# Kernel tuning notes

Hardware: AMD Instinct MI355X
Metric: run time of the kernel (lower is better)

## Reference

```python
import jax, jax.numpy as jnp
import numpy as np
from jax.scipy.linalg import expm

LATENT, HIDDEN, N_PARTS, K = 128, 2048, 128, 2048
OMEGA_DIM, TRANZ_DIM = 9 * N_PARTS, 3 * N_PARTS


def setup_inputs() -> dict:
    key = jax.random.key(0)
    ks = jax.random.split(key, 10)

    def w(k, out_d, in_d):
        # eqx.nn.Linear-style scale ~ 1/sqrt(fan_in)
        return jax.random.normal(k, (out_d, in_d), dtype=jnp.float32) / np.sqrt(in_d)

    return {
        "x_init": jax.random.normal(ks[0], (LATENT, K), dtype=jnp.float32),
        "Wo0": w(ks[1], HIDDEN, LATENT),
        "Wo1": w(ks[2], HIDDEN, HIDDEN),
        "Wo2": w(ks[3], HIDDEN, HIDDEN),
        "Wo3": w(ks[4], OMEGA_DIM, HIDDEN),
        "Wt0": w(ks[5], HIDDEN, LATENT),
        "Wt1": w(ks[6], HIDDEN, HIDDEN),
        "Wt2": w(ks[7], HIDDEN, HIDDEN),
        "Wt3": w(ks[8], TRANZ_DIM, HIDDEN),
    }


def _mlp(weights, x):
    # bias-free MLP, relu on all but last layer; x is (d_in, K)
    for i, W in enumerate(weights):
        x = W @ x
        if i + 1 < len(weights):
            x = jax.nn.relu(x)
    return x


def reference(x_init, Wo0, Wo1, Wo2, Wo3, Wt0, Wt1, Wt2, Wt3):
    omega = _mlp([Wo0, Wo1, Wo2, Wo3], x_init)            # (9n, K)
    n = omega.shape[0] // 9
    k = omega.shape[1]
    # exp_omega 2D branch: vmap over columns, each column -> (n,3,3) expm batch
    mats = omega.T.reshape(k * n, 3, 3)
    R = jax.vmap(expm)(mats).reshape(k, 9 * n)            # (K, 9n)
    rotations = R.T                                        # (9n, K)
    translations = _mlp([Wt0, Wt1, Wt2, Wt3], x_init)     # (3n, K)
    # form_transformations (2D branch): stack translation as a 4th row -> (12n, K)
    rot_r = rotations.reshape(n, 3, 3, k)
    tr_r = translations.reshape(n, 1, 3, k)
    transf = jnp.concatenate([rot_r, tr_r], axis=1).reshape(-1, k)  # (12n, K)
    return (omega, transf, rotations, translations)
```

## Files before the change

### kernel.cpp

```cpp
#include <hip/hip_runtime.h>
#include <stdint.h>


typedef short bf16x8 __attribute__((ext_vector_type(8)));
typedef float f32x4 __attribute__((ext_vector_type(4)));

__device__ __forceinline__ unsigned short f2bf(float f) {
  unsigned int x = __float_as_uint(f);
  unsigned int r = (x + 0x7fffu + ((x >> 16) & 1u)) >> 16;
  return (unsigned short)r;
}

__device__ __forceinline__ void gld_lds16(const void* g, void* l) {
  __builtin_amdgcn_global_load_lds(
      (__attribute__((address_space(1))) void*)(g),
      (__attribute__((address_space(3))) void*)(l),
      16, 0, 0);
}

__device__ __forceinline__ unsigned lds_addr(const void* p) {
  return (unsigned)(uintptr_t)(__attribute__((address_space(3))) const void*)p;
}

__device__ __forceinline__ bf16x8 ds_read128(unsigned a) {
  bf16x8 r;
  asm volatile("ds_read_b128 %0, %1" : "=v"(r) : "v"(a));
  return r;
}

#define ASM_BAR asm volatile("s_barrier" ::: "memory")
#define LGKM0   asm volatile("s_waitcnt lgkmcnt(0)" ::: "memory")
#define VMCNT0  asm volatile("s_waitcnt vmcnt(0)" ::: "memory")
#define SCHED0  __builtin_amdgcn_sched_barrier(0)

__global__ void prep_k(const float* __restrict__ x,
                       const float* __restrict__ wo0, const float* __restrict__ wo1,
                       const float* __restrict__ wo2, const float* __restrict__ wo3,
                       const float* __restrict__ wt0, const float* __restrict__ wt1,
                       const float* __restrict__ wt2, const float* __restrict__ wt3,
                       unsigned short* __restrict__ dst, unsigned short* __restrict__ xt) {
  __shared__ float tile[32][33];
  const int b = blockIdx.x;
  const int tid = threadIdx.x;
  if (b >= 9984) {
    const int r = b - 9984;
    const int bx = r & 63, by = r >> 6;
    const int tx = tid & 31, ty = tid >> 5;
#pragma unroll
    for (int i = 0; i < 32; i += 8)
      tile[ty + i][tx] = x[(size_t)(by * 32 + ty + i) * 2048 + bx * 32 + tx];
    __syncthreads();
#pragma unroll
    for (int i = 0; i < 32; i += 8)
      xt[(size_t)(bx * 32 + ty + i) * 128 + by * 32 + tx] = f2bf(tile[tx][ty + i]);
    return;
  }
  int idx = (b * 256 + tid) * 8;
  if (idx >= 20447232) return;
  const float* src;
  int off;
  if (idx < 8650752) {
    if (idx < 262144)       { src = wo0; off = idx; }
    else if (idx < 4456448) { src = wo1; off = idx - 262144; }
    else                    { src = wo2; off = idx - 4456448; }
  } else {
    if (idx < 11010048)      { src = wo3; off = idx - 8650752; }
    else if (idx < 11272192) { src = wt0; off = idx - 11010048; }
    else if (idx < 15466496) { src = wt1; off = idx - 11272192; }
    else if (idx < 19660800) { src = wt2; off = idx - 15466496; }
    else                     { src = wt3; off = idx - 19660800; }
  }
  float4 a = *(const float4*)(src + off);
  float4 c = *(const float4*)(src + off + 4);
  uint4 o;
  o.x = (unsigned)f2bf(a.x) | ((unsigned)f2bf(a.y) << 16);
  o.y = (unsigned)f2bf(a.z) | ((unsigned)f2bf(a.w) << 16);
  o.z = (unsigned)f2bf(c.x) | ((unsigned)f2bf(c.y) << 16);
  o.w = (unsigned)f2bf(c.z) | ((unsigned)f2bf(c.w) << 16);
  *(uint4*)(dst + idx) = o;
}

template <int SWZ>
__global__ __launch_bounds__(256, 2) void gemm_tn(
    const unsigned short* __restrict__ A0, const unsigned short* __restrict__ B0,
    unsigned short* __restrict__ C0, int n0tiles, int ldc0,
    const unsigned short* __restrict__ A1, const unsigned short* __restrict__ B1,
    unsigned short* __restrict__ C1, int ldc1, int K) {
  __shared__ alignas(16) unsigned short Asl[128 * 128];
  __shared__ alignas(16) unsigned short Bsl[128 * 128];

  int mt, yt;
  if (SWZ) {
    int id = blockIdx.x;
    int xcd = id & 7, s = id >> 3;
    mt = ((xcd & 1) << 3) + (s & 7);
    yt = ((xcd >> 1) << 3) + (s >> 3);
  } else {
    mt = blockIdx.x;
    yt = blockIdx.y;
  }

  const unsigned short* A;
  const unsigned short* B;
  unsigned short* C;
  int ldc;
  if (yt < n0tiles) { A = A0; B = B0; C = C0; ldc = ldc0; }
  else { A = A1; B = B1; C = C1; ldc = ldc1; yt -= n0tiles; }

  const unsigned short* Ab = A + (size_t)mt * 128 * K;
  const unsigned short* Bb = B + (size_t)yt * 128 * K;

  const int tid = threadIdx.x;
  const int wave = tid >> 6, lane = tid & 63;
  const int mw = (wave >> 1) * 64, nw = (wave & 1) * 64;
  const int l16 = lane & 15, quad = lane >> 4;

  f32x4 acc[4][4] = {};

  for (int k0 = 0; k0 < K; k0 += 128) {
#pragma unroll
    for (int i = 0; i < 8; ++i) {
      int c = i * 256 + tid;
      int row = c >> 4;
      int l = (c & 15) ^ (row & 15);
      gld_lds16(Ab + (size_t)row * K + k0 + l * 8, &Asl[c * 8]);
      gld_lds16(Bb + (size_t)row * K + k0 + l * 8, &Bsl[c * 8]);
    }
    __syncthreads();

#pragma unroll
    for (int h = 0; h < 4; ++h) {
      bf16x8 af[4], bfr[4];
#pragma unroll
      for (int t = 0; t < 4; ++t) {
        int row = mw + t * 16 + l16;
        int p = (h * 4 + quad) ^ (row & 15);
        af[t] = *(const bf16x8*)&Asl[row * 128 + p * 8];
      }
#pragma unroll
      for (int t = 0; t < 4; ++t) {
        int row = nw + t * 16 + l16;
        int p = (h * 4 + quad) ^ (row & 15);
        bfr[t] = *(const bf16x8*)&Bsl[row * 128 + p * 8];
      }
#pragma unroll
      for (int tm = 0; tm < 4; ++tm)
#pragma unroll
        for (int tn = 0; tn < 4; ++tn)
          acc[tm][tn] = __builtin_amdgcn_mfma_f32_16x16x32_bf16(af[tm], bfr[tn], acc[tm][tn], 0, 0, 0);
    }
    __syncthreads();
  }

  const int mbase = mt * 128 + mw;
  const int nbase = yt * 128 + nw;
#pragma unroll
  for (int tm = 0; tm < 4; ++tm) {
#pragma unroll
    for (int tn = 0; tn < 4; ++tn) {
      int col = nbase + tn * 16 + l16;
      int row0 = mbase + tm * 16 + quad * 4;
#pragma unroll
      for (int r = 0; r < 4; ++r) {
        float v = fmaxf(acc[tm][tn][r], 0.0f);
        C[(size_t)(row0 + r) * ldc + col] = f2bf(v);
      }
    }
  }
}

__global__ __launch_bounds__(256, 2) void gemm_db128(
    const unsigned short* __restrict__ A0, const unsigned short* __restrict__ B0,
    unsigned short* __restrict__ C0,
    const unsigned short* __restrict__ A1, const unsigned short* __restrict__ B1,
    unsigned short* __restrict__ C1, int K) {
  __shared__ alignas(16) unsigned short SM[2 * 16384];

  const int id = blockIdx.x;
  const int xcd = id & 7, s = id >> 3;
  const int mt = s & 15;
  const int ntt = xcd * 4 + (s >> 4);

  const unsigned short* A;
  const unsigned short* B;
  unsigned short* C;
  int ntl;
  if (ntt < 16) { A = A0; B = B0; C = C0; ntl = ntt; }
  else          { A = A1; B = B1; C = C1; ntl = ntt - 16; }

  const unsigned short* Ab = A + (size_t)mt * 128 * K;
  const unsigned short* Bb = B + (size_t)ntl * 128 * K;

  const int tid = threadIdx.x;
  const int wave = tid >> 6, lane = tid & 63;
  const int mw = (wave >> 1) * 64, nw = (wave & 1) * 64;
  const int l16 = lane & 15, quad = lane >> 4;

  const unsigned short* gA[4];
  const unsigned short* gB[4];
  int dAo[4], dBo[4];
#pragma unroll
  for (int i = 0; i < 4; ++i) {
    int c = i * 256 + tid;
    int row = c >> 3, pc = c & 7, l = pc ^ (row & 7);
    gA[i] = Ab + (size_t)row * K + l * 8;
    dAo[i] = c * 8;
    gB[i] = Bb + (size_t)row * K + l * 8;
    dBo[i] = 8192 + c * 8;
  }

  unsigned aoff[2][4], boff[2][4];
#pragma unroll
  for (int ph = 0; ph < 2; ++ph)
#pragma unroll
    for (int i = 0; i < 4; ++i) {
      int ra = mw + i * 16 + l16;
      aoff[ph][i] = (unsigned)(ra * 128 + (((ph * 4 + quad) ^ (ra & 7)) * 16));
      int rb = nw + i * 16 + l16;
      boff[ph][i] = (unsigned)(16384 + rb * 128 + (((ph * 4 + quad) ^ (rb & 7)) * 16));
    }
  const unsigned Au = lds_addr(SM);

  f32x4 acc[4][4] = {};
  const int NT = K >> 6;

  auto STAGE = [&](int slot, int k1) {
    const int so = slot * 16384;
#pragma unroll
    for (int i = 0; i < 4; ++i) gld_lds16(gA[i] + k1, SM + so + dAo[i]);
#pragma unroll
    for (int i = 0; i < 4; ++i) gld_lds16(gB[i] + k1, SM + so + dBo[i]);
  };

  STAGE(0, 0);
  VMCNT0;
  ASM_BAR;

  int cur = 0;
  for (int t = 0; t < NT; ++t) {
    int k1 = (t + 1) << 6;
    if (k1 > K - 64) k1 = K - 64;
    STAGE(cur ^ 1, k1);

    const unsigned base = Au + cur * 32768;
    bf16x8 a0[4], b0[4], a1[4], b1[4];
#pragma unroll
    for (int i = 0; i < 4; ++i) a0[i] = ds_read128(base + aoff[0][i]);
#pragma unroll
    for (int i = 0; i < 4; ++i) b0[i] = ds_read128(base + boff[0][i]);
#pragma unroll
    for (int i = 0; i < 4; ++i) a1[i] = ds_read128(base + aoff[1][i]);
#pragma unroll
    for (int i = 0; i < 4; ++i) b1[i] = ds_read128(base + boff[1][i]);
    LGKM0;
    SCHED0;
    __builtin_amdgcn_s_setprio(1);
#pragma unroll
    for (int tm = 0; tm < 4; ++tm)
#pragma unroll
      for (int tn = 0; tn < 4; ++tn)
        acc[tm][tn] = __builtin_amdgcn_mfma_f32_16x16x32_bf16(a0[tm], b0[tn], acc[tm][tn], 0, 0, 0);
#pragma unroll
    for (int tm = 0; tm < 4; ++tm)
#pragma unroll
      for (int tn = 0; tn < 4; ++tn)
        acc[tm][tn] = __builtin_amdgcn_mfma_f32_16x16x32_bf16(a1[tm], b1[tn], acc[tm][tn], 0, 0, 0);
    __builtin_amdgcn_s_setprio(0);
    SCHED0;

    VMCNT0;
    ASM_BAR;
    cur ^= 1;
  }

  const int mbase = mt * 128 + mw;
  const int nbase = ntl * 128 + nw;
#pragma unroll
  for (int tm = 0; tm < 4; ++tm) {
#pragma unroll
    for (int tn = 0; tn < 4; ++tn) {
      int col = nbase + tn * 16 + l16;
      int row0 = mbase + tm * 16 + quad * 4;
#pragma unroll
      for (int r = 0; r < 4; ++r) {
        float v = fmaxf(acc[tm][tn][r], 0.0f);
        C[(size_t)(row0 + r) * 2048 + col] = f2bf(v);
      }
    }
  }
}

__device__ __forceinline__ void mm3(const float* a, const float* b, float* c) {
#pragma unroll
  for (int r = 0; r < 3; ++r)
#pragma unroll
    for (int cc = 0; cc < 3; ++cc)
      c[r * 3 + cc] = a[r * 3 + 0] * b[0 + cc] + a[r * 3 + 1] * b[3 + cc] + a[r * 3 + 2] * b[6 + cc];
}

__device__ __forceinline__ void expm3(const float* a, float* E) {
  float n1 = 0.f;
#pragma unroll
  for (int c = 0; c < 3; ++c) {
    float s = fabsf(a[c]) + fabsf(a[3 + c]) + fabsf(a[6 + c]);
    n1 = fmaxf(n1, s);
  }
  int s = 0;
  if (n1 > 0.25f) {
    s = (int)ceilf(log2f(n1 * 4.0f));
    if (s < 0) s = 0;
  }
  const float scl = exp2f((float)(-s));
  float As[9];
#pragma unroll
  for (int i = 0; i < 9; ++i) As[i] = a[i] * scl;
  float T[9] = {1, 0, 0, 0, 1, 0, 0, 0, 1};
#pragma unroll
  for (int i = 0; i < 9; ++i) E[i] = T[i];
#pragma unroll
  for (int t = 1; t <= 12; ++t) {
    float Tn[9];
    mm3(T, As, Tn);
    const float inv = 1.0f / (float)t;
#pragma unroll
    for (int i = 0; i < 9; ++i) { T[i] = Tn[i] * inv; E[i] += T[i]; }
  }
  for (int q = 0; q < s; ++q) {
    float Tn[9];
    mm3(E, E, Tn);
#pragma unroll
    for (int i = 0; i < 9; ++i) E[i] = Tn[i];
  }
}

__global__ __launch_bounds__(256, 2) void gemm_l3(
    const unsigned short* __restrict__ Ho, const unsigned short* __restrict__ W9,
    const unsigned short* __restrict__ Ht, const unsigned short* __restrict__ W3,
    float* __restrict__ out) {
  __shared__ alignas(16) char smem[16384 + 39168];
  unsigned short* Asl = (unsigned short*)smem;
  unsigned short* Bsl = (unsigned short*)(smem + 16384);
  float* Cl = (float*)(smem + 16384);

  const int mt = blockIdx.x;
  const int yt = blockIdx.y;
  const int tid = threadIdx.x;
  const int wave = tid >> 6, lane = tid & 63;
  const int l16 = lane & 15, quad = lane >> 4;
  const int mbase = mt * 64;

  float* omega  = out;
  float* transf = out + (size_t)1152 * 2048;
  float* rot    = out + (size_t)(1152 + 1536) * 2048;
  float* transl = out + (size_t)(1152 + 1536 + 1152) * 2048;

  if (yt < 8) {
    const unsigned short* Ab = Ho + (size_t)mbase * 2048;
    const unsigned short* Bb = W9 + (size_t)yt * 144 * 2048;
    const int mw = wave * 16;
    f32x4 acc[9] = {};

    for (int k0 = 0; k0 < 2048; k0 += 128) {
#pragma unroll
      for (int i = 0; i < 4; ++i) {
        int c = i * 256 + tid;
        int row = c >> 4;
        int l = (c & 15) ^ (row & 15);
        gld_lds16(Ab + (size_t)row * 2048 + k0 + l * 8, &Asl[c * 8]);
      }
#pragma unroll
      for (int i = 0; i < 9; ++i) {
        int c = i * 256 + tid;
        int row = c >> 4;
        int l = (c & 15) ^ (row & 15);
        gld_lds16(Bb + (size_t)row * 2048 + k0 + l * 8, &Bsl[c * 8]);
      }
      __syncthreads();
#pragma unroll
      for (int h = 0; h < 4; ++h) {
        bf16x8 af;
        {
          int row = mw + l16;
          int p = (h * 4 + quad) ^ (row & 15);
          af = *(const bf16x8*)&Asl[row * 128 + p * 8];
        }
#pragma unroll
        for (int t = 0; t < 9; ++t) {
          int row = t * 16 + l16;
          int p = (h * 4 + quad) ^ (row & 15);
          bf16x8 bf = *(const bf16x8*)&Bsl[row * 128 + p * 8];
          acc[t] = __builtin_amdgcn_mfma_f32_16x16x32_bf16(af, bf, acc[t], 0, 0, 0);
        }
      }
      __syncthreads();
    }

#pragma unroll
    for (int t = 0; t < 9; ++t) {
      int d = t * 16 + l16;
      int s0 = mw + quad * 4;
      *(f32x4*)&Cl[d * 68 + s0] = acc[t];
    }
    __syncthreads();

    const int jbase = yt * 16;
    const int k = mbase + lane;
#pragma unroll 1
    for (int pp = 0; pp < 4; ++pp) {
      int pl = wave * 4 + pp;
      int j = jbase + pl;
      float a[9];
#pragma unroll
      for (int i = 0; i < 9; ++i) a[i] = Cl[(pl * 9 + i) * 68 + lane];
#pragma unroll
      for (int i = 0; i < 9; ++i) omega[(size_t)(9 * j + i) * 2048 + k] = a[i];
      float E[9];
      expm3(a, E);
#pragma unroll
      for (int i = 0; i < 9; ++i) {
        rot[(size_t)(9 * j + i) * 2048 + k] = E[i];
        transf[(size_t)(12 * j + i) * 2048 + k] = E[i];
      }
    }
  } else {
    const int nt = yt - 8;
    const unsigned short* Ab = Ht + (size_t)mbase * 2048;
    const unsigned short* Bb = W3 + (size_t)nt * 128 * 2048;
    const int mw = (wave >> 1) * 32, nw = (wave & 1) * 64;
    f32x4 acc[2][4] = {};

    for (int k0 = 0; k0 < 2048; k0 += 128) {
#pragma unroll
      for (int i = 0; i < 4; ++i) {
        int c = i * 256 + tid;
        int row = c >> 4;
        int l = (c & 15) ^ (row & 15);
        gld_lds16(Ab + (size_t)row * 2048 + k0 + l * 8, &Asl[c * 8]);
      }
#pragma unroll
      for (int i = 0; i < 8; ++i) {
        int c = i * 256 + tid;
        int row = c >> 4;
        int l = (c & 15) ^ (row & 15);
        gld_lds16(Bb + (size_t)row * 2048 + k0 + l * 8, &Bsl[c * 8]);
      }
      __syncthreads();
#pragma unroll
      for (int h = 0; h < 4; ++h) {
        bf16x8 af[2], bfr[4];
#pragma unroll
        for (int t = 0; t < 2; ++t) {
          int row = mw + t * 16 + l16;
          int p = (h * 4 + quad) ^ (row & 15);
          af[t] = *(const bf16x8*)&Asl[row * 128 + p * 8];
        }
#pragma unroll
        for (int t = 0; t < 4; ++t) {
          int row = nw + t * 16 + l16;
          int p = (h * 4 + quad) ^ (row & 15);
          bfr[t] = *(const bf16x8*)&Bsl[row * 128 + p * 8];
        }
#pragma unroll
        for (int tm = 0; tm < 2; ++tm)
#pragma unroll
          for (int tn = 0; tn < 4; ++tn)
            acc[tm][tn] = __builtin_amdgcn_mfma_f32_16x16x32_bf16(af[tm], bfr[tn], acc[tm][tn], 0, 0, 0);
      }
      __syncthreads();
    }

    const int nbase = nt * 128 + nw;
#pragma unroll
    for (int tm = 0; tm < 2; ++tm) {
#pragma unroll
      for (int tn = 0; tn < 4; ++tn) {
        int n = nbase + tn * 16 + l16;
        int row0 = mbase + mw + tm * 16 + quad * 4;
        int j = n / 3, c = n % 3;
        *(f32x4*)&transl[(size_t)n * 2048 + row0] = acc[tm][tn];
        *(f32x4*)&transf[(size_t)(12 * j + 9 + c) * 2048 + row0] = acc[tm][tn];
      }
    }
  }
}

extern "C" void kernel_launch(void* const* d_in, const int* in_sizes, int n_in,
                              void* d_out, int out_size, void* d_ws, size_t ws_size,
                              hipStream_t stream) {
  const float* x   = (const float*)d_in[0];
  const float* Wo0 = (const float*)d_in[1];
  const float* Wo1 = (const float*)d_in[2];
  const float* Wo2 = (const float*)d_in[3];
  const float* Wo3 = (const float*)d_in[4];
  const float* Wt0 = (const float*)d_in[5];
  const float* Wt1 = (const float*)d_in[6];
  const float* Wt2 = (const float*)d_in[7];
  const float* Wt3 = (const float*)d_in[8];

  unsigned short* wb   = (unsigned short*)d_ws;
  unsigned short* wo0b = wb + 0;
  unsigned short* wo1b = wb + 262144;
  unsigned short* wo2b = wb + 4456448;
  unsigned short* wo3b = wb + 8650752;
  unsigned short* wt0b = wb + 11010048;
  unsigned short* wt1b = wb + 11272192;
  unsigned short* wt2b = wb + 15466496;
  unsigned short* wt3b = wb + 19660800;
  unsigned short* Xt   = wb + 20447232;
  unsigned short* HoA  = Xt + 262144;
  unsigned short* HoB  = HoA + 4194304;
  unsigned short* HtA  = HoB + 4194304;
  unsigned short* HtB  = HtA + 4194304;

  prep_k<<<10240, 256, 0, stream>>>(x, Wo0, Wo1, Wo2, Wo3, Wt0, Wt1, Wt2, Wt3, wb, Xt);

  gemm_tn<1><<<512, 256, 0, stream>>>(Xt, wo0b, HoA, 16, 2048,
                                      Xt, wt0b, HtA, 2048, 128);
  gemm_db128<<<512, 256, 0, stream>>>(HoA, wo1b, HoB, HtA, wt1b, HtB, 2048);
  gemm_db128<<<512, 256, 0, stream>>>(HoB, wo2b, HoA, HtB, wt2b, HtA, 2048);
  gemm_l3<<<dim3(32, 11), 256, 0, stream>>>(HoA, wo3b, HtA, wt3b, (float*)d_out);
}
```

Measured before the change: 235.2 us.

## Double-buffer layer-3 GEMM LDS tiles with BK=64 prefetch pipeline

Restructures both branches of the final-layer GEMM (omega/expm and translation) to use a two-slot LDS ring with a K-step of 64. The next tile's global-to-LDS loads are issued before the current tile's MFMAs, replacing the single-buffer load/sync/compute loop with two __syncthreads per step. LDS addresses and swizzle offsets are precomputed with an 8-chunk XOR pattern, fragments are read with ds_read128, and the MFMA block is raised in priority. The aim is to hide global load latency behind matrix math. The cost is more register pressure for the precomputed offsets and fragments, and a redundant final prefetch.

New measurement: 234.6 us. Within noise of the previous version (-0.3%).

```diff
diff --git a/kernel.cpp b/kernel.cpp
--- a/kernel.cpp
+++ b/kernel.cpp
@@ -337,10 +337,8 @@
     const unsigned short* __restrict__ Ho, const unsigned short* __restrict__ W9,
     const unsigned short* __restrict__ Ht, const unsigned short* __restrict__ W3,
     float* __restrict__ out) {
-  __shared__ alignas(16) char smem[16384 + 39168];
-  unsigned short* Asl = (unsigned short*)smem;
-  unsigned short* Bsl = (unsigned short*)(smem + 16384);
-  float* Cl = (float*)(smem + 16384);
+  __shared__ alignas(16) unsigned short SM[26624];
+  float* Cl = (float*)SM;
 
   const int mt = blockIdx.x;
   const int yt = blockIdx.y;
@@ -354,45 +352,90 @@
   float* rot    = out + (size_t)(1152 + 1536) * 2048;
   float* transl = out + (size_t)(1152 + 1536 + 1152) * 2048;
 
+  const unsigned Au = lds_addr(SM);
+  const int NT = 32;
+
   if (yt < 8) {
     const unsigned short* Ab = Ho + (size_t)mbase * 2048;
     const unsigned short* Bb = W9 + (size_t)yt * 144 * 2048;
     const int mw = wave * 16;
     f32x4 acc[9] = {};
 
-    for (int k0 = 0; k0 < 2048; k0 += 128) {
-#pragma unroll
-      for (int i = 0; i < 4; ++i) {
-        int c = i * 256 + tid;
-        int row = c >> 4;
-        int l = (c & 15) ^ (row & 15);
-        gld_lds16(Ab + (size_t)row * 2048 + k0 + l * 8, &Asl[c * 8]);
-      }
-#pragma unroll
-      for (int i = 0; i < 9; ++i) {
-        int c = i * 256 + tid;
-        int row = c >> 4;
-        int l = (c & 15) ^ (row & 15);
-        gld_lds16(Bb + (size_t)row * 2048 + k0 + l * 8, &Bsl[c * 8]);
-      }
-      __syncthreads();
-#pragma unroll
-      for (int h = 0; h < 4; ++h) {
-        bf16x8 af;
-        {
-          int row = mw + l16;
-          int p = (h * 4 + quad) ^ (row & 15);
-          af = *(const bf16x8*)&Asl[row * 128 + p * 8];
-        }
-#pragma unroll
-        for (int t = 0; t < 9; ++t) {
-          int row = t * 16 + l16;
-          int p = (h * 4 + quad) ^ (row & 15);
-          bf16x8 bf = *(const bf16x8*)&Bsl[row * 128 + p * 8];
-          acc[t] = __builtin_amdgcn_mfma_f32_16x16x32_bf16(af, bf, acc[t], 0, 0, 0);
-        }
-      }
-      __syncthreads();
+    const unsigned short* gA[2];
+    int dAo[2];
+#pragma unroll
+    for (int i = 0; i < 2; ++i) {
+      int c = i * 256 + tid, row = c >> 3, pc = c & 7, l = pc ^ (row & 7);
+      gA[i] = Ab + (size_t)row * 2048 + l * 8;
+      dAo[i] = c * 8;
+    }
+    const unsigned short* gB[5];
+    int dBo[5];
+#pragma unroll
+    for (int i = 0; i < 5; ++i) {
+      int c = i * 256 + tid;
+      if (c > 1151) c = 1151;
+      int row = c >> 3, pc = c & 7, l = pc ^ (row & 7);
+      gB[i] = Bb + (size_t)row * 2048 + l * 8;
+      dBo[i] = 8192 + c * 8;
+    }
+    const bool b5 = (tid < 128);
+
+    auto STAGE = [&](int slot, int k1) {
+      const int sa = slot * 4096, sb = slot * 9216;
+#pragma unroll
+      for (int i = 0; i < 2; ++i) gld_lds16(gA[i] + k1, SM + sa + dAo[i]);
+#pragma unroll
+      for (int i = 0; i < 4; ++i) gld_lds16(gB[i] + k1, SM + sb + dBo[i]);
+      if (b5) gld_lds16(gB[4] + k1, SM + sb + dBo[4]);
+    };
+
+    unsigned aoff[2], boff[2][9];
+#pragma unroll
+    for (int ph = 0; ph < 2; ++ph) {
+      int ra = mw + l16;
+      aoff[ph] = (unsigned)(ra * 128 + (((ph * 4 + quad) ^ (ra & 7)) * 16));
+#pragma unroll
+      for (int t = 0; t < 9; ++t) {
+        int rb = t * 16 + l16;
+        boff[ph][t] = (unsigned)(16384 + rb * 128 + (((ph * 4 + quad) ^ (rb & 7)) * 16));
+      }
+    }
+
+    STAGE(0, 0);
+    VMCNT0;
+    ASM_BAR;
+
+    int cur = 0;
+    for (int t = 0; t < NT; ++t) {
+      int k1 = (t + 1) << 6;
+      if (k1 > 2048 - 64) k1 = 2048 - 64;
+      STAGE(cur ^ 1, k1);
+
+      const unsigned ab = Au + cur * 8192;
+      const unsigned bb = Au + cur * 18432;
+      bf16x8 af0, af1, bf0[9], bf1[9];
+      af0 = ds_read128(ab + aoff[0]);
+#pragma unroll
+      for (int i = 0; i < 9; ++i) bf0[i] = ds_read128(bb + boff[0][i]);
+      af1 = ds_read128(ab + aoff[1]);
+#pragma unroll
+      for (int i = 0; i < 9; ++i) bf1[i] = ds_read128(bb + boff[1][i]);
+      LGKM0;
+      SCHED0;
+      __builtin_amdgcn_s_setprio(1);
+#pragma unroll
+      for (int i = 0; i < 9; ++i)
+        acc[i] = __builtin_amdgcn_mfma_f32_16x16x32_bf16(af0, bf0[i], acc[i], 0, 0, 0);
+#pragma unroll
+      for (int i = 0; i < 9; ++i)
+        acc[i] = __builtin_amdgcn_mfma_f32_16x16x32_bf16(af1, bf1[i], acc[i], 0, 0, 0);
+      __builtin_amdgcn_s_setprio(0);
+      SCHED0;
+
+      VMCNT0;
+      ASM_BAR;
+      cur ^= 1;
     }
 
 #pragma unroll
@@ -429,44 +472,86 @@
     const int mw = (wave >> 1) * 32, nw = (wave & 1) * 64;
     f32x4 acc[2][4] = {};
 
-    for (int k0 = 0; k0 < 2048; k0 += 128) {
-#pragma unroll
-      for (int i = 0; i < 4; ++i) {
-        int c = i * 256 + tid;
-        int row = c >> 4;
-        int l = (c & 15) ^ (row & 15);
-        gld_lds16(Ab + (size_t)row * 2048 + k0 + l * 8, &Asl[c * 8]);
-      }
-#pragma unroll
-      for (int i = 0; i < 8; ++i) {
-        int c = i * 256 + tid;
-        int row = c >> 4;
-        int l = (c & 15) ^ (row & 15);
-        gld_lds16(Bb + (size_t)row * 2048 + k0 + l * 8, &Bsl[c * 8]);
-      }
-      __syncthreads();
-#pragma unroll
-      for (int h = 0; h < 4; ++h) {
-        bf16x8 af[2], bfr[4];
-#pragma unroll
-        for (int t = 0; t < 2; ++t) {
-          int row = mw + t * 16 + l16;
-          int p = (h * 4 + quad) ^ (row & 15);
-          af[t] = *(const bf16x8*)&Asl[row * 128 + p * 8];
-        }
-#pragma unroll
-        for (int t = 0; t < 4; ++t) {
-          int row = nw + t * 16 + l16;
-          int p = (h * 4 + quad) ^ (row & 15);
-          bfr[t] = *(const bf16x8*)&Bsl[row * 128 + p * 8];
-        }
-#pragma unroll
-        for (int tm = 0; tm < 2; ++tm)
-#pragma unroll
-          for (int tn = 0; tn < 4; ++tn)
-            acc[tm][tn] = __builtin_amdgcn_mfma_f32_16x16x32_bf16(af[tm], bfr[tn], acc[tm][tn], 0, 0, 0);
-      }
-      __syncthreads();
+    const unsigned short* gA[2];
+    int dAo[2];
+#pragma unroll
+    for (int i = 0; i < 2; ++i) {
+      int c = i * 256 + tid, row = c >> 3, pc = c & 7, l = pc ^ (row & 7);
+      gA[i] = Ab + (size_t)row * 2048 + l * 8;
+      dAo[i] = c * 8;
+    }
+    const unsigned short* gB[4];
+    int dBo[4];
+#pragma unroll
+    for (int i = 0; i < 4; ++i) {
+      int c = i * 256 + tid, row = c >> 3, pc = c & 7, l = pc ^ (row & 7);
+      gB[i] = Bb + (size_t)row * 2048 + l * 8;
+      dBo[i] = 8192 + c * 8;
+    }
+
+    auto STAGE = [&](int slot, int k1) {
+      const int sa = slot * 4096, sb = slot * 8192;
+#pragma unroll
+      for (int i = 0; i < 2; ++i) gld_lds16(gA[i] + k1, SM + sa + dAo[i]);
+#pragma unroll
+      for (int i = 0; i < 4; ++i) gld_lds16(gB[i] + k1, SM + sb + dBo[i]);
+    };
+
+    unsigned aoff[2][2], boff[2][4];
+#pragma unroll
+    for (int ph = 0; ph < 2; ++ph) {
+#pragma unroll
+      for (int t = 0; t < 2; ++t) {
+        int ra = mw + t * 16 + l16;
+        aoff[ph][t] = (unsigned)(ra * 128 + (((ph * 4 + quad) ^ (ra & 7)) * 16));
+      }
+#pragma unroll
+      for (int t = 0; t < 4; ++t) {
+        int rb = nw + t * 16 + l16;
+        boff[ph][t] = (unsigned)(16384 + rb * 128 + (((ph * 4 + quad) ^ (rb & 7)) * 16));
+      }
+    }
+
+    STAGE(0, 0);
+    VMCNT0;
+    ASM_BAR;
+
+    int cur = 0;
+    for (int t = 0; t < NT; ++t) {
+      int k1 = (t + 1) << 6;
+      if (k1 > 2048 - 64) k1 = 2048 - 64;
+      STAGE(cur ^ 1, k1);
+
+      const unsigned ab = Au + cur * 8192;
+      const unsigned bb = Au + cur * 16384;
+      bf16x8 a0[2], b0[4], a1[2], b1[4];
+#pragma unroll
+      for (int i = 0; i < 2; ++i) a0[i] = ds_read128(ab + aoff[0][i]);
+#pragma unroll
+      for (int i = 0; i < 4; ++i) b0[i] = ds_read128(bb + boff[0][i]);
+#pragma unroll
+      for (int i = 0; i < 2; ++i) a1[i] = ds_read128(ab + aoff[1][i]);
+#pragma unroll
+      for (int i = 0; i < 4; ++i) b1[i] = ds_read128(bb + boff[1][i]);
+      LGKM0;
+      SCHED0;
+      __builtin_amdgcn_s_setprio(1);
+#pragma unroll
+      for (int tm = 0; tm < 2; ++tm)
+#pragma unroll
+        for (int tn = 0; tn < 4; ++tn)
+          acc[tm][tn] = __builtin_amdgcn_mfma_f32_16x16x32_bf16(a0[tm], b0[tn], acc[tm][tn], 0, 0, 0);
+#pragma unroll
+      for (int tm = 0; tm < 2; ++tm)
+#pragma unroll
+        for (int tn = 0; tn < 4; ++tn)
+          acc[tm][tn] = __builtin_amdgcn_mfma_f32_16x16x32_bf16(a1[tm], b1[tn], acc[tm][tn], 0, 0, 0);
+      __builtin_amdgcn_s_setprio(0);
+      SCHED0;
+
+      VMCNT0;
+      ASM_BAR;
+      cur ^= 1;
     }
 
     const int nbase = nt * 128 + nw;
```

## Unify final-layer omega and translation GEMMs into one double-buffered kernel

Applied to the files above, without the earlier changes.

Replaces the branchy last-layer kernel, which used 8 omega blocks plus 3 translation blocks per M tile, with a single uniform kernel. Each block computes 144 omega columns and 48 translation columns together, so the grid shrinks to 32x8 and load imbalance between the two block types goes away. The K loop is now double-buffered in 64-wide steps, with async global-to-LDS loads overlapping the MFMA work, and it uses explicit ds_read, wait and setprio scheduling. In exchange, occupancy drops to one block per CU and the grid has fewer blocks.

After: 237.4 us. About the same (+0.9%).

```diff
diff --git a/kernel.cpp b/kernel.cpp
--- a/kernel.cpp
+++ b/kernel.cpp
@@ -333,19 +333,18 @@
   }
 }
 
-__global__ __launch_bounds__(256, 2) void gemm_l3(
+__global__ __launch_bounds__(256, 1) void gemm_l3u(
     const unsigned short* __restrict__ Ho, const unsigned short* __restrict__ W9,
     const unsigned short* __restrict__ Ht, const unsigned short* __restrict__ W3,
     float* __restrict__ out) {
-  __shared__ alignas(16) char smem[16384 + 39168];
-  unsigned short* Asl = (unsigned short*)smem;
-  unsigned short* Bsl = (unsigned short*)(smem + 16384);
-  float* Cl = (float*)(smem + 16384);
+  __shared__ alignas(16) unsigned short SM[40960];
+  float* Cl = (float*)SM;
 
   const int mt = blockIdx.x;
   const int yt = blockIdx.y;
   const int tid = threadIdx.x;
   const int wave = tid >> 6, lane = tid & 63;
+  const int wm = wave >> 1, wn = wave & 1;
   const int l16 = lane & 15, quad = lane >> 4;
   const int mbase = mt * 64;
 
@@ -354,132 +353,154 @@
   float* rot    = out + (size_t)(1152 + 1536) * 2048;
   float* transl = out + (size_t)(1152 + 1536 + 1152) * 2048;
 
-  if (yt < 8) {
-    const unsigned short* Ab = Ho + (size_t)mbase * 2048;
-    const unsigned short* Bb = W9 + (size_t)yt * 144 * 2048;
-    const int mw = wave * 16;
-    f32x4 acc[9] = {};
-
-    for (int k0 = 0; k0 < 2048; k0 += 128) {
-#pragma unroll
-      for (int i = 0; i < 4; ++i) {
-        int c = i * 256 + tid;
-        int row = c >> 4;
-        int l = (c & 15) ^ (row & 15);
-        gld_lds16(Ab + (size_t)row * 2048 + k0 + l * 8, &Asl[c * 8]);
+  const unsigned short* Ao  = Ho + (size_t)mbase * 2048;
+  const unsigned short* At  = Ht + (size_t)mbase * 2048;
+  const unsigned short* W9p = W9 + (size_t)yt * 144 * 2048;
+  const unsigned short* W3p = W3 + (size_t)yt * 48 * 2048;
+
+  const unsigned short* gAo[2];
+  const unsigned short* gAt[2];
+  int dA[2];
+#pragma unroll
+  for (int i = 0; i < 2; ++i) {
+    int c = i * 256 + tid, row = c >> 3, pc = c & 7, l = pc ^ (row & 7);
+    gAo[i] = Ao + (size_t)row * 2048 + l * 8;
+    gAt[i] = At + (size_t)row * 2048 + l * 8;
+    dA[i] = c * 8;
+  }
+  const unsigned short* gB[6];
+  int dB[6];
+#pragma unroll
+  for (int i = 0; i < 6; ++i) {
+    int c = i * 256 + tid, row = c >> 3, pc = c & 7, l = pc ^ (row & 7);
+    gB[i] = (row < 144 ? W9p + (size_t)row * 2048
+                       : W3p + (size_t)(row - 144) * 2048) + l * 8;
+    dB[i] = c * 8;
+  }
+
+  auto STAGE = [&](int s, int k1) {
+    const int ao = s * 4096, at = 8192 + s * 4096, bo = 16384 + s * 12288;
+#pragma unroll
+    for (int i = 0; i < 2; ++i) gld_lds16(gAo[i] + k1, SM + ao + dA[i]);
+#pragma unroll
+    for (int i = 0; i < 2; ++i) gld_lds16(gAt[i] + k1, SM + at + dA[i]);
+#pragma unroll
+    for (int i = 0; i < 6; ++i) gld_lds16(gB[i] + k1, SM + bo + dB[i]);
+  };
+
+  unsigned aoff[2][2], boff[2][6];
+#pragma unroll
+  for (int ph = 0; ph < 2; ++ph) {
+#pragma unroll
+    for (int tm = 0; tm < 2; ++tm) {
+      int ra = wm * 32 + tm * 16 + l16;
+      aoff[ph][tm] = (unsigned)(ra * 128 + (((ph * 4 + quad) ^ (ra & 7)) * 16));
+    }
+#pragma unroll
+    for (int tb = 0; tb < 6; ++tb) {
+      int rb = (wn * 6 + tb) * 16 + l16;
+      boff[ph][tb] = (unsigned)(rb * 128 + (((ph * 4 + quad) ^ (rb & 7)) * 16));
+    }
+  }
+  const unsigned Au = lds_addr(SM);
+
+  f32x4 acc[2][6] = {};
+
+  STAGE(0, 0);
+  VMCNT0;
+  ASM_BAR;
+
+  int cur = 0;
+  for (int t = 0; t < 32; ++t) {
+    int k1 = (t + 1) << 6;
+    if (k1 > 2048 - 64) k1 = 2048 - 64;
+    STAGE(cur ^ 1, k1);
+
+    const unsigned aoB = Au + cur * 8192;
+    const unsigned atB = Au + 16384 + cur * 8192;
+    const unsigned bB  = Au + 32768 + cur * 24576;
+    bf16x8 a0o[2], a1o[2], a0t[2], a1t[2], b0[6], b1[6];
+#pragma unroll
+    for (int i = 0; i < 2; ++i) {
+      a0o[i] = ds_read128(aoB + aoff[0][i]);
+      a1o[i] = ds_read128(aoB + aoff[1][i]);
+    }
+    if (wn) {
+#pragma unroll
+      for (int i = 0; i < 2; ++i) {
+        a0t[i] = ds_read128(atB + aoff[0][i]);
+        a1t[i] = ds_read128(atB + aoff[1][i]);
       }
-#pragma unroll
-      for (int i = 0; i < 9; ++i) {
-        int c = i * 256 + tid;
-        int row = c >> 4;
-        int l = (c & 15) ^ (row & 15);
-        gld_lds16(Bb + (size_t)row * 2048 + k0 + l * 8, &Bsl[c * 8]);
+    }
+#pragma unroll
+    for (int i = 0; i < 6; ++i) {
+      b0[i] = ds_read128(bB + boff[0][i]);
+      b1[i] = ds_read128(bB + boff[1][i]);
+    }
+    LGKM0;
+    SCHED0;
+    if (!wn) {
+#pragma unroll
+      for (int i = 0; i < 2; ++i) { a0t[i] = a0o[i]; a1t[i] = a1o[i]; }
+    }
+    __builtin_amdgcn_s_setprio(1);
+#pragma unroll
+    for (int tm = 0; tm < 2; ++tm)
+#pragma unroll
+      for (int tb = 0; tb < 6; ++tb)
+        acc[tm][tb] = __builtin_amdgcn_mfma_f32_16x16x32_bf16(
+            tb >= 3 ? a0t[tm] : a0o[tm], b0[tb], acc[tm][tb], 0, 0, 0);
+#pragma unroll
+    for (int tm = 0; tm < 2; ++tm)
+#pragma unroll
+      for (int tb = 0; tb < 6; ++tb)
+        acc[tm][tb] = __builtin_amdgcn_mfma_f32_16x16x32_bf16(
+            tb >= 3 ? a1t[tm] : a1o[tm], b1[tb], acc[tm][tb], 0, 0, 0);
+    __builtin_amdgcn_s_setprio(0);
+    SCHED0;
+
+    VMCNT0;
+    ASM_BAR;
+    cur ^= 1;
+  }
+
+#pragma unroll
+  for (int tm = 0; tm < 2; ++tm) {
+#pragma unroll
+    for (int tb = 0; tb < 6; ++tb) {
+      int st = wn * 6 + tb;
+      int s0 = wm * 32 + tm * 16 + quad * 4;
+      if (st < 9) {
+        int d = st * 16 + l16;
+        *(f32x4*)&Cl[d * 68 + s0] = acc[tm][tb];
+      } else {
+        int n = yt * 48 + (st - 9) * 16 + l16;
+        int row0 = mbase + s0;
+        int j = n / 3, c2 = n % 3;
+        *(f32x4*)&transl[(size_t)n * 2048 + row0] = acc[tm][tb];
+        *(f32x4*)&transf[(size_t)(12 * j + 9 + c2) * 2048 + row0] = acc[tm][tb];
       }
-      __syncthreads();
-#pragma unroll
-      for (int h = 0; h < 4; ++h) {
-        bf16x8 af;
-        {
-          int row = mw + l16;
-          int p = (h * 4 + quad) ^ (row & 15);
-          af = *(const bf16x8*)&Asl[row * 128 + p * 8];
-        }
-#pragma unroll
-        for (int t = 0; t < 9; ++t) {
-          int row = t * 16 + l16;
-          int p = (h * 4 + quad) ^ (row & 15);
-          bf16x8 bf = *(const bf16x8*)&Bsl[row * 128 + p * 8];
-          acc[t] = __builtin_amdgcn_mfma_f32_16x16x32_bf16(af, bf, acc[t], 0, 0, 0);
-        }
-      }
-      __syncthreads();
-    }
-
-#pragma unroll
-    for (int t = 0; t < 9; ++t) {
-      int d = t * 16 + l16;
-      int s0 = mw + quad * 4;
-      *(f32x4*)&Cl[d * 68 + s0] = acc[t];
-    }
-    __syncthreads();
-
-    const int jbase = yt * 16;
-    const int k = mbase + lane;
+    }
+  }
+  __syncthreads();
+
+  const int jbase = yt * 16;
+  const int k = mbase + lane;
 #pragma unroll 1
-    for (int pp = 0; pp < 4; ++pp) {
-      int pl = wave * 4 + pp;
-      int j = jbase + pl;
-      float a[9];
-#pragma unroll
-      for (int i = 0; i < 9; ++i) a[i] = Cl[(pl * 9 + i) * 68 + lane];
-#pragma unroll
-      for (int i = 0; i < 9; ++i) omega[(size_t)(9 * j + i) * 2048 + k] = a[i];
-      float E[9];
-      expm3(a, E);
-#pragma unroll
-      for (int i = 0; i < 9; ++i) {
-        rot[(size_t)(9 * j + i) * 2048 + k] = E[i];
-        transf[(size_t)(12 * j + i) * 2048 + k] = E[i];
-      }
-    }
-  } else {
-    const int nt = yt - 8;
-    const unsigned short* Ab = Ht + (size_t)mbase * 2048;
-    const unsigned short* Bb = W3 + (size_t)nt * 128 * 2048;
-    const int mw = (wave >> 1) * 32, nw = (wave & 1) * 64;
-    f32x4 acc[2][4] = {};
-
-    for (int k0 = 0; k0 < 2048; k0 += 128) {
-#pragma unroll
-      for (int i = 0; i < 4; ++i) {
-        int c = i * 256 + tid;
-        int row = c >> 4;
-        int l = (c & 15) ^ (row & 15);
-        gld_lds16(Ab + (size_t)row * 2048 + k0 + l * 8, &Asl[c * 8]);
-      }
-#pragma unroll
-      for (int i = 0; i < 8; ++i) {
-        int c = i * 256 + tid;
-        int row = c >> 4;
-        int l = (c & 15) ^ (row & 15);
-        gld_lds16(Bb + (size_t)row * 2048 + k0 + l * 8, &Bsl[c * 8]);
-      }
-      __syncthreads();
-#pragma unroll
-      for (int h = 0; h < 4; ++h) {
-        bf16x8 af[2], bfr[4];
-#pragma unroll
-        for (int t = 0; t < 2; ++t) {
-          int row = mw + t * 16 + l16;
-          int p = (h * 4 + quad) ^ (row & 15);
-          af[t] = *(const bf16x8*)&Asl[row * 128 + p * 8];
-        }
-#pragma unroll
-        for (int t = 0; t < 4; ++t) {
-          int row = nw + t * 16 + l16;
-          int p = (h * 4 + quad) ^ (row & 15);
-          bfr[t] = *(const bf16x8*)&Bsl[row * 128 + p * 8];
-        }
-#pragma unroll
-        for (int tm = 0; tm < 2; ++tm)
-#pragma unroll
-          for (int tn = 0; tn < 4; ++tn)
-            acc[tm][tn] = __builtin_amdgcn_mfma_f32_16x16x32_bf16(af[tm], bfr[tn], acc[tm][tn], 0, 0, 0);
-      }
-      __syncthreads();
-    }
-
-    const int nbase = nt * 128 + nw;
-#pragma unroll
-    for (int tm = 0; tm < 2; ++tm) {
-#pragma unroll
-      for (int tn = 0; tn < 4; ++tn) {
-        int n = nbase + tn * 16 + l16;
-        int row0 = mbase + mw + tm * 16 + quad * 4;
-        int j = n / 3, c = n % 3;
-        *(f32x4*)&transl[(size_t)n * 2048 + row0] = acc[tm][tn];
-        *(f32x4*)&transf[(size_t)(12 * j + 9 + c) * 2048 + row0] = acc[tm][tn];
-      }
+  for (int pp = 0; pp < 4; ++pp) {
+    int pl = wave * 4 + pp;
+    int j = jbase + pl;
+    float a[9];
+#pragma unroll
+    for (int i = 0; i < 9; ++i) a[i] = Cl[(pl * 9 + i) * 68 + lane];
+#pragma unroll
+    for (int i = 0; i < 9; ++i) omega[(size_t)(9 * j + i) * 2048 + k] = a[i];
+    float E[9];
+    expm3(a, E);
+#pragma unroll
+    for (int i = 0; i < 9; ++i) {
+      rot[(size_t)(9 * j + i) * 2048 + k] = E[i];
+      transf[(size_t)(12 * j + i) * 2048 + k] = E[i];
     }
   }
 }
@@ -518,5 +539,5 @@
                                       Xt, wt0b, HtA, 2048, 128);
   gemm_db128<<<512, 256, 0, stream>>>(HoA, wo1b, HoB, HtA, wt1b, HtB, 2048);
   gemm_db128<<<512, 256, 0, stream>>>(HoB, wo2b, HoA, HtB, wt2b, HtA, 2048);
-  gemm_l3<<<dim3(32, 11), 256, 0, stream>>>(HoA, wo3b, HtA, wt3b, (float*)d_out);
-}
+  gemm_l3u<<<dim3(32, 8), 256, 0, stream>>>(HoA, wo3b, HtA, wt3b, (float*)d_out);
+}
```
